# Kernel tuning notes

Measured on AMD Instinct MI355X. Metric: run time of the kernel, lower is better.

## Reference

```python
import jax, jax.numpy as jnp
import numpy as np

B, T, D = 4, 2048, 2048
H = 16
HD = D // H  # head_dim = 128


def setup_inputs() -> dict:
    key = jax.random.key(0)
    ks = jax.random.split(key, 10)
    s = 0.02
    return {
        "x": jax.random.normal(ks[0], (B, T, D), dtype=jnp.float32),
        "Wq": jax.random.normal(ks[1], (D, D), dtype=jnp.float32) * s,
        "bq": jnp.zeros((D,), dtype=jnp.float32),
        "Wk": jax.random.normal(ks[2], (D, D), dtype=jnp.float32) * s,
        "bk": jnp.zeros((D,), dtype=jnp.float32),
        "Wv": jax.random.normal(ks[3], (D, D), dtype=jnp.float32) * s,
        "bv": jnp.zeros((D,), dtype=jnp.float32),
        "Wo": jax.random.normal(ks[4], (D, D), dtype=jnp.float32) * s,
        "bo": jnp.zeros((D,), dtype=jnp.float32),
    }


def reference(x, Wq, bq, Wk, bk, Wv, bv, Wo, bo):
    b, t, _ = x.shape
    # projections (nn.Linear: x @ W.T + b); split heads -> (b, h, t, hd)
    def split_heads(y):
        return y.reshape(b, t, H, HD).transpose(0, 2, 1, 3)

    q = split_heads(x @ Wq.T + bq)
    k = split_heads(x @ Wk.T + bk)
    v = split_heads(x @ Wv.T + bv)

    scale = 1.0 / jnp.sqrt(jnp.float32(HD))
    scores = jnp.einsum("bhqd,bhkd->bhqk", q, k) * scale  # (b,h,t,t)
    causal = jnp.triu(jnp.ones((t, t), dtype=bool), k=1)
    scores = jnp.where(causal, -jnp.inf, scores)
    attn = jax.nn.softmax(scores, axis=-1)
    # dropout p=0.0 -> identity
    ctx = jnp.einsum("bhqk,bhkd->bhqd", attn, v)  # (b,h,t,hd)
    ctx = ctx.transpose(0, 2, 1, 3).reshape(b, t, D)
    return ctx @ Wo.T + bo
```

## Files before the change

kernel.cpp:

```cpp
#include <hip/hip_runtime.h>
#include <hip/hip_bf16.h>

typedef __attribute__((ext_vector_type(8))) __bf16 bf16x8;
typedef __attribute__((ext_vector_type(4))) __bf16 bf16x4;
typedef __attribute__((ext_vector_type(4))) short s16x4;
typedef __attribute__((ext_vector_type(4))) float f32x4;
typedef unsigned int u32;

#define LOG2E 1.4426950408889634f

__device__ __forceinline__ void gload_lds16(const void* g, void* l) {
  __builtin_amdgcn_global_load_lds(
      (const __attribute__((address_space(1))) u32*)g,
      (__attribute__((address_space(3))) u32*)l, 16, 0, 0);
}

__global__ __launch_bounds__(256)
void cvt_f32_bf16(const float* __restrict__ src, __hip_bfloat16* __restrict__ dst, int n4) {
  int i = blockIdx.x * blockDim.x + threadIdx.x;
  if (i < n4) {
    float4 v = ((const float4*)src)[i];
    union { unsigned long long u; __hip_bfloat16 h[4]; } o;
    o.h[0] = __float2bfloat16(v.x);
    o.h[1] = __float2bfloat16(v.y);
    o.h[2] = __float2bfloat16(v.z);
    o.h[3] = __float2bfloat16(v.w);
    ((unsigned long long*)dst)[i] = o.u;
  }
}

__global__ __launch_bounds__(256)
void cvt_all(const float* __restrict__ x,
             const float* __restrict__ w0, const float* __restrict__ w1,
             const float* __restrict__ w2, const float* __restrict__ w3,
             __hip_bfloat16* __restrict__ xb,
             __hip_bfloat16* __restrict__ b0, __hip_bfloat16* __restrict__ b1,
             __hip_bfloat16* __restrict__ b2, __hip_bfloat16* __restrict__ b3,
             int n4x, int n4wlog)
{
  int i = blockIdx.x * blockDim.x + threadIdx.x;
  const float* src; __hip_bfloat16* dst; int off;
  if (i < n4x) { src = x; dst = xb; off = i; }
  else {
    int j = i - n4x;
    int which = j >> n4wlog;
    off = j & ((1 << n4wlog) - 1);
    src = which == 0 ? w0 : which == 1 ? w1 : which == 2 ? w2 : w3;
    dst = which == 0 ? b0 : which == 1 ? b1 : which == 2 ? b2 : b3;
  }
  float4 v = ((const float4*)src)[off];
  union { unsigned long long u; __hip_bfloat16 h[4]; } o;
  o.h[0] = __float2bfloat16(v.x);
  o.h[1] = __float2bfloat16(v.y);
  o.h[2] = __float2bfloat16(v.z);
  o.h[3] = __float2bfloat16(v.w);
  ((unsigned long long*)dst)[off] = o.u;
}

#define VMW(N) asm volatile("s_waitcnt vmcnt(" #N ")" ::: "memory")

#define GPHASE(P, MH, NH, RDA, RDB, ISSUE, WAITC, LGHINT)                      \
  {                                                                            \
    if (RDA) {                                                                 \
      _Pragma("unroll")                                                        \
      for (int i = 0; i < 4; ++i) {                                            \
        const char* pa = Ab + (((MH) * 128 + wr * 64 + i * 16 + l15) << 7);    \
        afr[i][0] = *(const bf16x8*)(pa + ph0);                                \
        afr[i][1] = *(const bf16x8*)(pa + ph1);                                \
      }                                                                        \
    }                                                                          \
    if (RDB) {                                                                 \
      _Pragma("unroll")                                                        \
      for (int j = 0; j < 2; ++j) {                                            \
        const char* pb = Bb + (((NH) * 128 + wc * 32 + j * 16 + l15) << 7);    \
        bfr[j][0] = *(const bf16x8*)(pb + ph0);                                \
        bfr[j][1] = *(const bf16x8*)(pb + ph1);                                \
      }                                                                        \
    }                                                                          \
    ISSUE;                                                                     \
    WAITC;                                                                     \
    LGHINT;                                                                    \
    __builtin_amdgcn_s_barrier();                                              \
    asm volatile("s_waitcnt lgkmcnt(0)" ::: "memory");                         \
    __builtin_amdgcn_sched_barrier(0);                                         \
    __builtin_amdgcn_s_setprio(1);                                             \
    _Pragma("unroll")                                                          \
    for (int ks = 0; ks < 2; ++ks)                                             \
      _Pragma("unroll")                                                        \
      for (int i = 0; i < 4; ++i)                                              \
        _Pragma("unroll")                                                      \
        for (int j = 0; j < 2; ++j)                                            \
          acc[P][i][j] = __builtin_amdgcn_mfma_f32_16x16x32_bf16(              \
              afr[i][ks], bfr[j][ks], acc[P][i][j], 0, 0, 0);                  \
    __builtin_amdgcn_s_setprio(0);                                             \
    __builtin_amdgcn_s_barrier();                                              \
  }

template<int MODE>
__global__ __launch_bounds__(512, 2)
void gemm256(const __hip_bfloat16* __restrict__ A,
             const __hip_bfloat16* __restrict__ W,
             const float* __restrict__ bias,
             __hip_bfloat16* __restrict__ C,
             float* __restrict__ Cf,
             int M, int N, int K, float oscale)
{
  __shared__ __align__(16) __hip_bfloat16 SH[2][32768];

  const int tid = threadIdx.x;
  const int lane = tid & 63;
  const int w = tid >> 6;
  const int wr = w >> 2, wc = w & 3;
  const int quad = lane >> 4, l15 = lane & 15;

  const int nb = N >> 8;
  const int swz = (blockIdx.x & 7) * ((int)gridDim.x >> 3) + ((int)blockIdx.x >> 3);
  const int m0 = (swz / nb) << 8;
  const int n0 = (swz % nb) << 8;

  const int NT = K >> 6;

  const int r0 = tid >> 3;
  const int kb = ((tid & 7) ^ (r0 & 7)) << 3;
  const __hip_bfloat16* Ag = A + (size_t)(m0 + r0) * K + kb;
  const __hip_bfloat16* Wg = W + (size_t)(n0 + r0) * K + kb;

  const int ph0 = (quad ^ (l15 & 7)) << 4;
  const int ph1 = ((4 + quad) ^ (l15 & 7)) << 4;

  f32x4 acc[4][4][2] = {};
  bf16x8 afr[4][2], bfr[2][2];

  auto issueA = [&](int t2, int mh) {
    if (t2 < NT) {
      const __hip_bfloat16* g = Ag + (size_t)(mh * 128) * K + (t2 << 6);
      char* l = (char*)SH[t2 & 1] + mh * 16384 + (tid << 4);
      gload_lds16(g, l);
      gload_lds16(g + (size_t)64 * K, l + 8192);
    }
  };
  auto issueB = [&](int t2, int nh) {
    if (t2 < NT) {
      const __hip_bfloat16* g = Wg + (size_t)(nh * 128) * K + (t2 << 6);
      char* l = (char*)SH[t2 & 1] + 32768 + nh * 16384 + (tid << 4);
      gload_lds16(g, l);
      gload_lds16(g + (size_t)64 * K, l + 8192);
    }
  };

  issueA(0, 0); issueB(0, 0); issueB(0, 1); issueA(0, 1);
  VMW(4);
  __builtin_amdgcn_s_barrier();

  for (int t = 0; t < NT; ++t) {
    const char* Ab = (const char*)SH[t & 1];
    const char* Bb = Ab + 32768;
    const bool more = (t + 1 < NT);

    GPHASE(0, 0, 0, true, true, issueA(t + 1, 0),
           if (more) { VMW(4); } else { VMW(2); },
           asm volatile("s_waitcnt lgkmcnt(8)" ::: "memory"));
    GPHASE(1, 0, 1, false, true, issueB(t + 1, 0),
           if (more) { VMW(4); } else { VMW(0); }, );
    GPHASE(2, 1, 1, true, false, issueB(t + 1, 1), , );
    GPHASE(3, 1, 0, false, true, issueA(t + 1, 1),
           if (more) { VMW(4); }, );
  }

#pragma unroll
  for (int p = 0; p < 4; ++p) {
    const int mh = (p >= 2) ? 1 : 0;
    const int nh = (p == 1 || p == 2) ? 1 : 0;
#pragma unroll
    for (int i = 0; i < 4; ++i) {
      int mbase = m0 + mh * 128 + wr * 64 + i * 16 + quad * 4;
#pragma unroll
      for (int j = 0; j < 2; ++j) {
        int n = n0 + nh * 128 + wc * 32 + j * 16 + l15;
        float bv = bias[n];
#pragma unroll
        for (int r = 0; r < 4; ++r) {
          int mm = mbase + r;
          float v = (acc[p][i][j][r] + bv) * oscale;
          if (MODE == 0) {
            C[(size_t)mm * N + n] = __float2bfloat16(v);
          } else if (MODE == 1) {
            int b = mm >> 11, tt = mm & 2047;
            C[((size_t)(b * 2048 + n)) * 2048 + tt] = __float2bfloat16(v);
          } else {
            Cf[(size_t)mm * N + n] = v;
          }
        }
      }
    }
  }
}

__global__ __launch_bounds__(256, 2)
void attn_fwd(const __hip_bfloat16* __restrict__ Q,
              const __hip_bfloat16* __restrict__ K,
              const __hip_bfloat16* __restrict__ Vt,
              __hip_bfloat16* __restrict__ ctx)
{
  __shared__ __align__(16) __hip_bfloat16 KVl[2][16384];

  const int tid = threadIdx.x;
  const int lane = tid & 63;
  const int w = tid >> 6;
  const int quad = lane >> 4, l15 = lane & 15;
  const int bid = blockIdx.x;
  const int qi = 15 - (bid >> 6);
  const int bh = bid & 63;
  const int b = bh >> 4, h = bh & 15;
  const int q0 = qi * 128;

  bf16x8 qf[2][4];
  for (int sub = 0; sub < 2; ++sub) {
    const __hip_bfloat16* qp =
        Q + ((size_t)(b * 2048 + q0 + sub * 64 + w * 16 + l15)) * 2048 + h * 128 + quad * 8;
    for (int ks = 0; ks < 4; ++ks) qf[sub][ks] = *(const bf16x8*)(qp + ks * 32);
  }

  int krow[4], kcol[4], vrow[4], vcol[4], soff[4];
  for (int p = 0; p < 4; ++p) {
    int off = (tid + p * 256) * 16;
    soff[p] = off;
    int r1 = off >> 8;
    int pc1 = (off >> 4) & 15;
    krow[p] = r1; kcol[p] = ((pc1 & 8) | ((pc1 & 7) ^ (r1 & 7))) * 8;
    int r2 = off >> 7;
    int pc2 = (off >> 4) & 7;
    vrow[p] = r2; vcol[p] = (pc2 ^ (r2 & 7)) * 8;
  }

  f32x4 o[2][8] = {};
  float lsum[2] = {0.f, 0.f};
  const int base0 = q0 + w * 16;
  const int base1 = q0 + 64 + w * 16;

  const int ktmax = (q0 + 127) >> 6;

  for (int p = 0; p < 4; ++p)
    gload_lds16(K + ((size_t)(b * 2048 + krow[p])) * 2048 + h * 128 + kcol[p],
                (char*)&KVl[0][0] + soff[p]);
  for (int p = 0; p < 4; ++p)
    gload_lds16(Vt + ((size_t)(b * 2048 + h * 128 + vrow[p])) * 2048 + vcol[p],
                (char*)&KVl[0][8192] + soff[p]);
  __syncthreads();

  for (int kt = 0; kt <= ktmax; ++kt) {
    const int cur = kt & 1;
    const int kbase = kt * 64;
    if (kt < ktmax) {
      const int nbase = kbase + 64;
      for (int p = 0; p < 4; ++p)
        gload_lds16(K + ((size_t)(b * 2048 + nbase + krow[p])) * 2048 + h * 128 + kcol[p],
                    (char*)&KVl[1 - cur][0] + soff[p]);
      for (int p = 0; p < 4; ++p)
        gload_lds16(Vt + ((size_t)(b * 2048 + h * 128 + vrow[p])) * 2048 + nbase + vcol[p],
                    (char*)&KVl[1 - cur][8192] + soff[p]);
    }

    const char* Kl = (const char*)&KVl[cur][0];
    const char* Vl = (const char*)&KVl[cur][8192];

    const bool act0 = kbase <= base0 + 15;
    const bool act1 = kbase <= base1 + 15;

    f32x4 s[2][4] = {};
#pragma unroll
    for (int ct = 0; ct < 4; ++ct) {
      int row = ct * 16 + l15;
#pragma unroll
      for (int ks = 0; ks < 4; ++ks) {
        int c = ks * 4 + quad;
        int ph = (c & 8) | ((c & 7) ^ (row & 7));
        bf16x8 kf = *(const bf16x8*)(Kl + row * 256 + ph * 16);
        if (act0) s[0][ct] = __builtin_amdgcn_mfma_f32_16x16x32_bf16(kf, qf[0][ks], s[0][ct], 0, 0, 0);
        if (act1) s[1][ct] = __builtin_amdgcn_mfma_f32_16x16x32_bf16(kf, qf[1][ks], s[1][ct], 0, 0, 0);
      }
    }

    union pu { bf16x4 h[2]; bf16x8 v; };
    pu pf8[2][2];
#pragma unroll
    for (int sub = 0; sub < 2; ++sub) {
      if (!(sub ? act1 : act0)) continue;
      const int bs = sub ? base1 : base0;
      const bool full = (kbase + 63 <= bs);
      float lsv = lsum[sub];
#pragma unroll
      for (int ct = 0; ct < 4; ++ct) {
        bf16x4 pb;
        if (full) {
#pragma unroll
          for (int r = 0; r < 4; ++r) {
            float e = exp2f(s[sub][ct][r]);
            lsv += e; pb[r] = (__bf16)e;
          }
        } else {
          int diff = (bs + l15) - (kbase + ct * 16 + quad * 4);
#pragma unroll
          for (int r = 0; r < 4; ++r) {
            float e = (r <= diff) ? exp2f(s[sub][ct][r]) : 0.f;
            lsv += e; pb[r] = (__bf16)e;
          }
        }
        pf8[sub][ct >> 1].h[ct & 1] = pb;
      }
      lsum[sub] = lsv;
    }

    const int h8 = (quad & 1) * 8;
    const int qh = quad >> 1;
#pragma unroll
    for (int dgrp = 0; dgrp < 8; ++dgrp) {
      int row = dgrp * 16 + l15;
      int rx = row & 7;
      const char* vrow_p = Vl + row * 128;
#pragma unroll
      for (int c = 0; c < 2; ++c) {
        int ch1 = 4 * c + qh;
        union { struct { s16x4 a, b; } s; bf16x8 v; } vu;
        vu.s.a = *(const s16x4*)(vrow_p + ((ch1 ^ rx) * 16) + h8);
        vu.s.b = *(const s16x4*)(vrow_p + (((ch1 + 2) ^ rx) * 16) + h8);
        if (act0) o[0][dgrp] = __builtin_amdgcn_mfma_f32_16x16x32_bf16(vu.v, pf8[0][c].v, o[0][dgrp], 0, 0, 0);
        if (act1) o[1][dgrp] = __builtin_amdgcn_mfma_f32_16x16x32_bf16(vu.v, pf8[1][c].v, o[1][dgrp], 0, 0, 0);
      }
    }
    __syncthreads();
  }

  for (int sub = 0; sub < 2; ++sub) {
    float ls = lsum[sub];
    ls += __shfl_xor(ls, 16, 64);
    ls += __shfl_xor(ls, 32, 64);
    lsum[sub] = 1.0f / ls;
  }

  for (int sub = 0; sub < 2; ++sub) {
    char* rb = (char*)&KVl[0][0] + (w * 2 + sub) * 4096;
    float inv = lsum[sub];
    for (int dgrp = 0; dgrp < 8; ++dgrp) {
      for (int rp = 0; rp < 2; ++rp) {
        __hip_bfloat16 lo = __float2bfloat16(o[sub][dgrp][rp * 2] * inv);
        __hip_bfloat16 hi = __float2bfloat16(o[sub][dgrp][rp * 2 + 1] * inv);
        u32 pk = (u32)*(unsigned short*)&lo | ((u32)*(unsigned short*)&hi << 16);
        int c = dgrp * 2 + (quad >> 1);
        int cp = c ^ (l15 & 7);
        *(u32*)(rb + l15 * 256 + cp * 16 + (quad & 1) * 8 + rp * 4) = pk;
      }
    }
    int q2 = lane & 15;
    int qq = q0 + sub * 64 + w * 16 + q2;
    __hip_bfloat16* cp = ctx + ((size_t)(b * 2048 + qq)) * 2048 + h * 128;
    for (int rr = 0; rr < 4; ++rr) {
      int cl = quad + rr * 4;
      int cph = cl ^ (q2 & 7);
      uint4 val = *(const uint4*)(rb + q2 * 256 + cph * 16);
      *(uint4*)(cp + cl * 8) = val;
    }
  }
}

extern "C" void kernel_launch(void* const* d_in, const int* in_sizes, int n_in,
                              void* d_out, int out_size, void* d_ws, size_t ws_size,
                              hipStream_t stream)
{
  (void)in_sizes; (void)n_in; (void)out_size;
  const float* x  = (const float*)d_in[0];
  const float* Wq = (const float*)d_in[1];
  const float* bq = (const float*)d_in[2];
  const float* Wk = (const float*)d_in[3];
  const float* bk = (const float*)d_in[4];
  const float* Wv = (const float*)d_in[5];
  const float* bv = (const float*)d_in[6];
  const float* Wo = (const float*)d_in[7];
  const float* bo = (const float*)d_in[8];
  float* out = (float*)d_out;

  const int M = 8192, D = 2048;
  const size_t MD = (size_t)M * D, DD = (size_t)D * D;
  const int n4x = (int)(MD / 4), n4w = (int)(DD / 4);
  dim3 cb(256), bb(256), ga(1024);
  dim3 gg((M / 256) * (D / 256)), gbb(512);
  const float qscale = 0.08838834764831845f * LOG2E;

  if (ws_size >= (4 * MD + 4 * DD) * 2) {
    __hip_bfloat16* xb  = (__hip_bfloat16*)d_ws;
    __hip_bfloat16* Wqb = xb  + MD;
    __hip_bfloat16* Wkb = Wqb + DD;
    __hip_bfloat16* Wvb = Wkb + DD;
    __hip_bfloat16* Wob = Wvb + DD;
    __hip_bfloat16* Qb  = Wob + DD;
    __hip_bfloat16* Kb  = Qb  + MD;
    __hip_bfloat16* Vtb = Kb  + MD;
    __hip_bfloat16* Cx  = xb;

    int tot4 = n4x + 4 * n4w;
    hipLaunchKernelGGL(cvt_all, dim3(tot4 / 256), cb, 0, stream,
                       x, Wq, Wk, Wv, Wo, xb, Wqb, Wkb, Wvb, Wob, n4x, 20);
    hipLaunchKernelGGL((gemm256<0>), gg, gbb, 0, stream, xb, Wqb, bq, Qb, (float*)nullptr, M, D, D, qscale);
    hipLaunchKernelGGL((gemm256<0>), gg, gbb, 0, stream, xb, Wkb, bk, Kb, (float*)nullptr, M, D, D, 1.0f);
    hipLaunchKernelGGL((gemm256<1>), gg, gbb, 0, stream, xb, Wvb, bv, Vtb, (float*)nullptr, M, D, D, 1.0f);
    hipLaunchKernelGGL(attn_fwd, ga, bb, 0, stream, Qb, Kb, Vtb, Cx);
    hipLaunchKernelGGL((gemm256<2>), gg, gbb, 0, stream, Cx, Wob, bo, (__hip_bfloat16*)nullptr, out, M, D, D, 1.0f);
  } else {
    __hip_bfloat16* xb  = (__hip_bfloat16*)d_ws;
    __hip_bfloat16* Wb  = xb  + MD;
    __hip_bfloat16* Qb  = Wb  + DD;
    __hip_bfloat16* Kb  = Qb  + MD;
    __hip_bfloat16* Vtb = Kb  + MD;
    __hip_bfloat16* Cx  = xb;

    dim3 cgx((n4x + 255) / 256), cgw((n4w + 255) / 256);
    hipLaunchKernelGGL(cvt_f32_bf16, cgx, cb, 0, stream, x, xb, n4x);
    hipLaunchKernelGGL(cvt_f32_bf16, cgw, cb, 0, stream, Wq, Wb, n4w);
    hipLaunchKernelGGL((gemm256<0>), gg, gbb, 0, stream, xb, Wb, bq, Qb, (float*)nullptr, M, D, D, qscale);
    hipLaunchKernelGGL(cvt_f32_bf16, cgw, cb, 0, stream, Wk, Wb, n4w);
    hipLaunchKernelGGL((gemm256<0>), gg, gbb, 0, stream, xb, Wb, bk, Kb, (float*)nullptr, M, D, D, 1.0f);
    hipLaunchKernelGGL(cvt_f32_bf16, cgw, cb, 0, stream, Wv, Wb, n4w);
    hipLaunchKernelGGL((gemm256<1>), gg, gbb, 0, stream, xb, Wb, bv, Vtb, (float*)nullptr, M, D, D, 1.0f);
    hipLaunchKernelGGL(attn_fwd, ga, bb, 0, stream, Qb, Kb, Vtb, Cx);
    hipLaunchKernelGGL(cvt_f32_bf16, cgw, cb, 0, stream, Wo, Wb, n4w);
    hipLaunchKernelGGL((gemm256<2>), gg, gbb, 0, stream, Cx, Wb, bo, (__hip_bfloat16*)nullptr, out, M, D, D, 1.0f);
  }
}
```

Measured before the change: 533.7 us.

## Restructure GEMM main loop to cache B fragments and drop per-phase trailing barriers

Replaces the GPHASE macro in the 256x256 bf16 GEMM with four explicit phases. The B-half-0 fragments are now kept in registers (b0fr) and reused in phase 3 instead of being re-read from LDS. Each phase now waits on global loads, hits a single barrier, and then reads LDS. This removes the trailing barrier, the explicit lgkmcnt waits and the sched_barrier, cutting LDS traffic and synchronisation per K-step. In exchange it uses more VGPRs for the extra fragment set, and it gives up the hand-tuned scheduling, leaving overlap of LDS reads with MFMA to the compiler.

New measurement: 544.8 us. +2.1%, slower.

```diff
diff --git a/kernel.cpp b/kernel.cpp
--- a/kernel.cpp
+++ b/kernel.cpp
@@ -59,43 +59,6 @@
 
 #define VMW(N) asm volatile("s_waitcnt vmcnt(" #N ")" ::: "memory")
 
-#define GPHASE(P, MH, NH, RDA, RDB, ISSUE, WAITC, LGHINT)                      \
-  {                                                                            \
-    if (RDA) {                                                                 \
-      _Pragma("unroll")                                                        \
-      for (int i = 0; i < 4; ++i) {                                            \
-        const char* pa = Ab + (((MH) * 128 + wr * 64 + i * 16 + l15) << 7);    \
-        afr[i][0] = *(const bf16x8*)(pa + ph0);                                \
-        afr[i][1] = *(const bf16x8*)(pa + ph1);                                \
-      }                                                                        \
-    }                                                                          \
-    if (RDB) {                                                                 \
-      _Pragma("unroll")                                                        \
-      for (int j = 0; j < 2; ++j) {                                            \
-        const char* pb = Bb + (((NH) * 128 + wc * 32 + j * 16 + l15) << 7);    \
-        bfr[j][0] = *(const bf16x8*)(pb + ph0);                                \
-        bfr[j][1] = *(const bf16x8*)(pb + ph1);                                \
-      }                                                                        \
-    }                                                                          \
-    ISSUE;                                                                     \
-    WAITC;                                                                     \
-    LGHINT;                                                                    \
-    __builtin_amdgcn_s_barrier();                                              \
-    asm volatile("s_waitcnt lgkmcnt(0)" ::: "memory");                         \
-    __builtin_amdgcn_sched_barrier(0);                                         \
-    __builtin_amdgcn_s_setprio(1);                                             \
-    _Pragma("unroll")                                                          \
-    for (int ks = 0; ks < 2; ++ks)                                             \
-      _Pragma("unroll")                                                        \
-      for (int i = 0; i < 4; ++i)                                              \
-        _Pragma("unroll")                                                      \
-        for (int j = 0; j < 2; ++j)                                            \
-          acc[P][i][j] = __builtin_amdgcn_mfma_f32_16x16x32_bf16(              \
-              afr[i][ks], bfr[j][ks], acc[P][i][j], 0, 0, 0);                  \
-    __builtin_amdgcn_s_setprio(0);                                             \
-    __builtin_amdgcn_s_barrier();                                              \
-  }
-
 template<int MODE>
 __global__ __launch_bounds__(512, 2)
 void gemm256(const __hip_bfloat16* __restrict__ A,
@@ -129,7 +92,7 @@
   const int ph1 = ((4 + quad) ^ (l15 & 7)) << 4;
 
   f32x4 acc[4][4][2] = {};
-  bf16x8 afr[4][2], bfr[2][2];
+  bf16x8 afr[4][2], b0fr[2][2], b1fr[2][2];
 
   auto issueA = [&](int t2, int mh) {
     if (t2 < NT) {
@@ -157,14 +120,85 @@
     const char* Bb = Ab + 32768;
     const bool more = (t + 1 < NT);
 
-    GPHASE(0, 0, 0, true, true, issueA(t + 1, 0),
-           if (more) { VMW(4); } else { VMW(2); },
-           asm volatile("s_waitcnt lgkmcnt(8)" ::: "memory"));
-    GPHASE(1, 0, 1, false, true, issueB(t + 1, 0),
-           if (more) { VMW(4); } else { VMW(0); }, );
-    GPHASE(2, 1, 1, true, false, issueB(t + 1, 1), , );
-    GPHASE(3, 1, 0, false, true, issueA(t + 1, 1),
-           if (more) { VMW(4); }, );
+    issueA(t + 1, 0);
+    if (more) { VMW(4); } else { VMW(2); }
+    __builtin_amdgcn_s_barrier();
+#pragma unroll
+    for (int j = 0; j < 2; ++j) {
+      const char* pb = Bb + ((wc * 32 + j * 16 + l15) << 7);
+      b0fr[j][0] = *(const bf16x8*)(pb + ph0);
+      b0fr[j][1] = *(const bf16x8*)(pb + ph1);
+    }
+#pragma unroll
+    for (int i = 0; i < 4; ++i) {
+      const char* pa = Ab + ((wr * 64 + i * 16 + l15) << 7);
+      afr[i][0] = *(const bf16x8*)(pa + ph0);
+      afr[i][1] = *(const bf16x8*)(pa + ph1);
+    }
+    __builtin_amdgcn_s_setprio(1);
+#pragma unroll
+    for (int ks = 0; ks < 2; ++ks)
+#pragma unroll
+      for (int i = 0; i < 4; ++i)
+#pragma unroll
+        for (int j = 0; j < 2; ++j)
+          acc[0][i][j] = __builtin_amdgcn_mfma_f32_16x16x32_bf16(
+              afr[i][ks], b0fr[j][ks], acc[0][i][j], 0, 0, 0);
+    __builtin_amdgcn_s_setprio(0);
+
+    issueB(t + 1, 0);
+    if (more) { VMW(4); } else { VMW(0); }
+    __builtin_amdgcn_s_barrier();
+#pragma unroll
+    for (int j = 0; j < 2; ++j) {
+      const char* pb = Bb + ((128 + wc * 32 + j * 16 + l15) << 7);
+      b1fr[j][0] = *(const bf16x8*)(pb + ph0);
+      b1fr[j][1] = *(const bf16x8*)(pb + ph1);
+    }
+    __builtin_amdgcn_s_setprio(1);
+#pragma unroll
+    for (int ks = 0; ks < 2; ++ks)
+#pragma unroll
+      for (int i = 0; i < 4; ++i)
+#pragma unroll
+        for (int j = 0; j < 2; ++j)
+          acc[1][i][j] = __builtin_amdgcn_mfma_f32_16x16x32_bf16(
+              afr[i][ks], b1fr[j][ks], acc[1][i][j], 0, 0, 0);
+    __builtin_amdgcn_s_setprio(0);
+
+    issueB(t + 1, 1);
+    if (more) { VMW(4); }
+    __builtin_amdgcn_s_barrier();
+#pragma unroll
+    for (int i = 0; i < 4; ++i) {
+      const char* pa = Ab + ((128 + wr * 64 + i * 16 + l15) << 7);
+      afr[i][0] = *(const bf16x8*)(pa + ph0);
+      afr[i][1] = *(const bf16x8*)(pa + ph1);
+    }
+    __builtin_amdgcn_s_setprio(1);
+#pragma unroll
+    for (int ks = 0; ks < 2; ++ks)
+#pragma unroll
+      for (int i = 0; i < 4; ++i)
+#pragma unroll
+        for (int j = 0; j < 2; ++j)
+          acc[2][i][j] = __builtin_amdgcn_mfma_f32_16x16x32_bf16(
+              afr[i][ks], b1fr[j][ks], acc[2][i][j], 0, 0, 0);
+    __builtin_amdgcn_s_setprio(0);
+
+    issueA(t + 1, 1);
+    if (more) { VMW(4); }
+    __builtin_amdgcn_s_barrier();
+    __builtin_amdgcn_s_setprio(1);
+#pragma unroll
+    for (int ks = 0; ks < 2; ++ks)
+#pragma unroll
+      for (int i = 0; i < 4; ++i)
+#pragma unroll
+        for (int j = 0; j < 2; ++j)
+          acc[3][i][j] = __builtin_amdgcn_mfma_f32_16x16x32_bf16(
+              afr[i][ks], b0fr[j][ks], acc[3][i][j], 0, 0, 0);
+    __builtin_amdgcn_s_setprio(0);
   }
 
 #pragma unroll
```
